# Performance work log

Hardware: AMD Instinct MI355X
Metric: run time of the kernel (lower is better)

Reference implementation:

```python
import jax, jax.numpy as jnp
import numpy as np
from jax import lax

# Config constants (DeepSeek-V2-style gate)
N_EXPERTS = 64
TOP_K = 6
N_GROUP = 8
TOPK_GROUP = 3
NORM_TOPK_PROB = True
ROUTED_SCALING_FACTOR = 1.0


def setup_inputs() -> dict:
    key = jax.random.key(0)
    k1, k2 = jax.random.split(key)
    B, S, H = 4, 8192, 2048
    hidden_states = jax.random.normal(k1, (B, S, H), dtype=jnp.float32)
    # gate kernel: (n_routed_experts, gating_dim), kaiming-uniform-ish scale
    bound = float(np.sqrt(6.0 / H))
    kernel = jax.random.uniform(k2, (N_EXPERTS, H), dtype=jnp.float32, minval=-bound, maxval=bound)
    return {"hidden_states": hidden_states, "kernel": kernel}


def reference(hidden_states, kernel):
    B, S, H = hidden_states.shape
    T = B * S
    flat = hidden_states.reshape(T, H).astype(jnp.float32)
    # logits: [T, E]  (x @ W^T, as in DeepSeek gate)
    logits = jnp.einsum("th,eh->te", flat, kernel.astype(jnp.float32))
    scores = jax.nn.softmax(logits, axis=-1)  # [T, E]

    # group_limited_greedy: pick best TOPK_GROUP groups per token, mask the rest
    per_group = N_EXPERTS // N_GROUP
    group_scores = scores.reshape(T, N_GROUP, per_group).max(axis=-1)  # [T, G]
    top_group_idx = lax.top_k(group_scores, TOPK_GROUP)[1]  # [T, topk_group]
    group_mask = jnp.zeros((T, N_GROUP), dtype=scores.dtype)
    group_mask = group_mask.at[jnp.arange(T)[:, None], top_group_idx].set(1.0)
    score_mask = jnp.repeat(group_mask[:, :, None], per_group, axis=2).reshape(T, N_EXPERTS)
    masked_scores = jnp.where(score_mask.astype(bool), scores, 0.0)
    topk_weight, _ = lax.top_k(masked_scores, TOP_K)  # [T, top_k]

    if TOP_K > 1 and NORM_TOPK_PROB:
        denom = jnp.sum(topk_weight, axis=-1, keepdims=True) + 1e-20
        topk_weight = topk_weight / denom
    else:
        topk_weight = topk_weight * ROUTED_SCALING_FACTOR
    return topk_weight
```

## Files before the change

### kernel.cpp

```cpp
#include <hip/hip_runtime.h>
#include <hip/hip_bf16.h>


#define HD 2048
#define NE 64
#define NCH 16
#define BUFB 32768

typedef __attribute__((ext_vector_type(4))) float f4;
typedef __attribute__((ext_vector_type(8))) short s8;
typedef __attribute__((ext_vector_type(8))) _Float16 h8;
typedef __attribute__((ext_vector_type(4))) float accv;
typedef unsigned short u16;

__device__ __forceinline__ void split8h(const f4 v0, const f4 v1, s8& h, s8& l) {
  #pragma unroll
  for (int i = 0; i < 8; ++i) {
    float a = (i < 4) ? v0[i] : v1[i - 4];
    _Float16 hh = (_Float16)a;
    float r = a - (float)hh;
    _Float16 ll = (_Float16)r;
    h[i] = __builtin_bit_cast(short, hh);
    l[i] = __builtin_bit_cast(short, ll);
  }
}

__device__ __forceinline__ accv mfma3(s8 ah, s8 al, s8 bh, s8 bl, accv t) {
  h8 AH = __builtin_bit_cast(h8, ah);
  h8 AL = __builtin_bit_cast(h8, al);
  h8 BH = __builtin_bit_cast(h8, bh);
  h8 BL = __builtin_bit_cast(h8, bl);
  t = __builtin_amdgcn_mfma_f32_16x16x32_f16(AH, BH, t, 0, 0, 0);
  t = __builtin_amdgcn_mfma_f32_16x16x32_f16(AH, BL, t, 0, 0, 0);
  t = __builtin_amdgcn_mfma_f32_16x16x32_f16(AL, BH, t, 0, 0, 0);
  return t;
}

__device__ __forceinline__ void epilogue64(const float* v, float* op) {
  float gm[8];
  #pragma unroll
  for (int g = 0; g < 8; ++g) {
    float mx = v[g * 8];
    #pragma unroll
    for (int j = 1; j < 8; ++j) mx = fmaxf(mx, v[g * 8 + j]);
    gm[g] = mx;
  }
  unsigned selmask = 0u;
  #pragma unroll
  for (int itg = 0; itg < 3; ++itg) {
    float best = gm[0];
    #pragma unroll
    for (int g = 1; g < 8; ++g) best = fmaxf(best, gm[g]);
    int bi = 7;
    #pragma unroll
    for (int g = 6; g >= 0; --g)
      if (gm[g] == best) bi = g;
    selmask |= (1u << bi);
    #pragma unroll
    for (int g = 0; g < 8; ++g) gm[g] = (g == bi) ? -3.0e38f : gm[g];
  }
  float t0 = -3.0e38f, t1 = -3.0e38f, t2 = -3.0e38f;
  float t3 = -3.0e38f, t4 = -3.0e38f, t5 = -3.0e38f;
  #pragma unroll
  for (int g = 0; g < 8; ++g) {
    const bool sel = (selmask >> g) & 1u;
    #pragma unroll
    for (int j = 0; j < 8; ++j) {
      float x = sel ? v[g * 8 + j] : -3.0e38f;
      float mm;
      mm = fmaxf(t0, x); x = fminf(t0, x); t0 = mm;
      mm = fmaxf(t1, x); x = fminf(t1, x); t1 = mm;
      mm = fmaxf(t2, x); x = fminf(t2, x); t2 = mm;
      mm = fmaxf(t3, x); x = fminf(t3, x); t3 = mm;
      mm = fmaxf(t4, x); x = fminf(t4, x); t4 = mm;
      t5 = fmaxf(t5, x);
    }
  }
  float e0 = 1.0f;
  float e1 = __expf(t1 - t0);
  float e2 = __expf(t2 - t0);
  float e3 = __expf(t3 - t0);
  float e4 = __expf(t4 - t0);
  float e5 = __expf(t5 - t0);
  float sum = e0 + e1 + e2 + e3 + e4 + e5;
  float inv = 1.0f / sum;
  op[0] = e0 * inv; op[1] = e1 * inv; op[2] = e2 * inv;
  op[3] = e3 * inv; op[4] = e4 * inv; op[5] = e5 * inv;
}

__global__ __launch_bounds__(64) void cvtW2(const float* __restrict__ Wf,
                                            u16* __restrict__ Wh,
                                            u16* __restrict__ Wl) {
  int i = (blockIdx.x * 64 + threadIdx.x) * 8;
  f4 v0 = *(const f4*)(Wf + i);
  f4 v1 = *(const f4*)(Wf + i + 4);
  s8 h, l;
  split8h(v0, v1, h, l);
  *(s8*)((short*)Wh + i) = h;
  *(s8*)((short*)Wl + i) = l;
}

template <bool PRE>
__global__ __launch_bounds__(512, 4) void gateF(
    const float* __restrict__ X, const float* __restrict__ Wf,
    const u16* __restrict__ Wh, const u16* __restrict__ Wl,
    float* __restrict__ out) {
  __shared__ __align__(16) unsigned char smem[2 * BUFB];

  const int tid = threadIdx.x;
  const int lane = tid & 63;
  const int w = tid >> 6;
  const int ec = lane & 15;
  const int kg = lane >> 4;
  const int tok0 = blockIdx.x * 128;

  const float* pA = X + (size_t)(tok0 + w * 16 + ec) * HD + kg * 8;

  const int sw = w >> 1, spl = w & 1;
  const u16* Wsrc = spl ? Wl : Wh;
  const size_t wsrcb = (size_t)ec * HD + sw * 32 + kg * 8;
  const int sdstb = sw * 8192 + spl * 4096 + lane * 16;

  accv acc[4];
  #pragma unroll
  for (int f = 0; f < 4; ++f) acc[f] = (accv){0.f, 0.f, 0.f, 0.f};

  f4 ar[4][2];

  if constexpr (PRE) {
    #pragma unroll
    for (int j = 0; j < 4; ++j) {
      const size_t o = wsrcb + (size_t)j * 16 * HD;
      __builtin_amdgcn_global_load_lds((const unsigned int*)(Wsrc + o),
                                       (unsigned int*)(smem + sdstb + j * 1024), 16, 0, 0);
    }
  } else {
    #pragma unroll
    for (int j = 0; j < 4; ++j) {
      const size_t o = wsrcb + (size_t)j * 16 * HD;
      f4 r0 = *(const f4*)(Wf + o);
      f4 r1 = *(const f4*)(Wf + o + 4);
      s8 th, tl;
      split8h(r0, r1, th, tl);
      *(s8*)(smem + sw * 8192 + j * 1024 + lane * 16) = th;
      *(s8*)(smem + sw * 8192 + 4096 + j * 1024 + lane * 16) = tl;
    }
  }
  __builtin_amdgcn_sched_barrier(0);
  #pragma unroll
  for (int st = 0; st < 4; ++st) {
    ar[st][0] = *(const f4*)(pA + st * 32);
    ar[st][1] = *(const f4*)(pA + st * 32 + 4);
  }
  __builtin_amdgcn_sched_barrier(0);
  if constexpr (PRE) {
    asm volatile("s_waitcnt vmcnt(8) lgkmcnt(0)");
  } else {
    asm volatile("s_waitcnt lgkmcnt(0)");
  }
  __builtin_amdgcn_s_barrier();
  __builtin_amdgcn_sched_barrier(0);


  for (int c = 0; c < NCH; ++c) {
    const unsigned char* rb = smem + (c & 1) * BUFB;
    unsigned char* wb = smem + ((c + 1) & 1) * BUFB;
    const bool do_stage = (c + 1 < NCH);

    f4 q0[4], q1[4];
    if (do_stage) {
      if constexpr (PRE) {
        #pragma unroll
        for (int j = 0; j < 4; ++j) {
          const size_t o = wsrcb + (size_t)j * 16 * HD + (size_t)(c + 1) * 128;
          __builtin_amdgcn_global_load_lds((const unsigned int*)(Wsrc + o),
                                           (unsigned int*)(wb + sdstb + j * 1024), 16, 0, 0);
        }
      } else {
        #pragma unroll
        for (int j = 0; j < 4; ++j) {
          const size_t o = wsrcb + (size_t)j * 16 * HD + (size_t)(c + 1) * 128;
          q0[j] = *(const f4*)(Wf + o);
          q1[j] = *(const f4*)(Wf + o + 4);
        }
      }
    }
    __builtin_amdgcn_sched_barrier(0);

    #pragma unroll
    for (int st = 0; st < 4; ++st) {
      const int t = c * 4 + st;
      s8 ah, al;
      split8h(ar[st][0], ar[st][1], ah, al);
      const int tn = (t + 4 < 64) ? (t + 4) : 63;
      ar[st][0] = *(const f4*)(pA + tn * 32);
      ar[st][1] = *(const f4*)(pA + tn * 32 + 4);
      #pragma unroll
      for (int f = 0; f < 4; ++f) {
        const unsigned char* bp = rb + st * 8192 + f * 1024 + lane * 16;
        s8 bh = *(const s8*)(bp);
        s8 bl = *(const s8*)(bp + 4096);
        acc[f] = mfma3(ah, al, bh, bl, acc[f]);
      }
    }

    if (do_stage) {
      if constexpr (!PRE) {
        #pragma unroll
        for (int j = 0; j < 4; ++j) {
          s8 th, tl;
          split8h(q0[j], q1[j], th, tl);
          *(s8*)(wb + sw * 8192 + j * 1024 + lane * 16) = th;
          *(s8*)(wb + sw * 8192 + 4096 + j * 1024 + lane * 16) = tl;
        }
      }
    }
    if (do_stage) {
      __builtin_amdgcn_sched_barrier(0);
      if constexpr (PRE) {
        asm volatile("s_waitcnt vmcnt(8) lgkmcnt(0)");
      } else {
        asm volatile("s_waitcnt lgkmcnt(0)");
      }
      __builtin_amdgcn_s_barrier();
      __builtin_amdgcn_sched_barrier(0);
    }
  }

  __syncthreads();
  float* lf = (float*)smem + w * 1088;
  #pragma unroll
  for (int f = 0; f < 4; ++f)
    #pragma unroll
    for (int r = 0; r < 4; ++r)
      lf[(kg * 4 + r) * 68 + f * 16 + ec] = acc[f][r];

  if (lane < 16) {
    float v[64];
    #pragma unroll
    for (int i = 0; i < 16; ++i) {
      f4 q = *(const f4*)(lf + lane * 68 + 4 * i);
      v[4 * i + 0] = q.x; v[4 * i + 1] = q.y;
      v[4 * i + 2] = q.z; v[4 * i + 3] = q.w;
    }
    epilogue64(v, out + (size_t)(tok0 + w * 16 + lane) * 6);
  }
}

extern "C" void kernel_launch(void* const* d_in, const int* in_sizes, int n_in,
                              void* d_out, int out_size, void* d_ws, size_t ws_size,
                              hipStream_t stream) {
  const float* X = (const float*)d_in[0];
  const float* Wf = (const float*)d_in[1];
  float* out = (float*)d_out;
  const int T = in_sizes[0] / HD;
  const int nblk = T / 128;

  const size_t need = (size_t)NE * HD * sizeof(u16);
  if (ws_size >= 2 * need) {
    u16* Whi = (u16*)d_ws;
    u16* Wlo = Whi + (size_t)NE * HD;
    cvtW2<<<dim3(256), dim3(64), 0, stream>>>(Wf, Whi, Wlo);
    gateF<true><<<dim3(nblk), dim3(512), 0, stream>>>(X, Wf, Whi, Wlo, out);
  } else {
    gateF<false><<<dim3(nblk), dim3(512), 0, stream>>>(X, Wf, nullptr, nullptr, out);
  }
}
```

Measured before the change: 70.85 us.

## Stream activations through per-wave swizzled LDS ring via direct global-to-LDS loads

Activation tiles no longer go through register prefetch. Each wave now issues global_load_lds into a 4-slot XOR-swizzled LDS ring, three k-steps ahead, with fine-grained vmcnt waits, and reads its operands back from LDS. LDS grows to 128 KB, so occupancy is capped at 2 blocks per CU, and s_setprio is raised around the MFMA section. The aim is to free VGPRs and hide global latency better, at the cost of lower occupancy and fragile vmcnt bookkeeping. The non-PRE path also changes: each wave now writes only one half of the split weights, which looks like a behaviour change.

```diff
diff --git a/kernel.cpp b/kernel.cpp
--- a/kernel.cpp
+++ b/kernel.cpp
@@ -5,7 +5,9 @@
 #define HD 2048
 #define NE 64
 #define NCH 16
-#define BUFB 32768
+#define ABASE 0
+#define BBASE 65536
+#define BBUF 32768
 
 typedef __attribute__((ext_vector_type(4))) float f4;
 typedef __attribute__((ext_vector_type(8))) short s8;
@@ -101,11 +103,11 @@
 }
 
 template <bool PRE>
-__global__ __launch_bounds__(512, 4) void gateF(
+__global__ __launch_bounds__(512, 2) void gateF(
     const float* __restrict__ X, const float* __restrict__ Wf,
     const u16* __restrict__ Wh, const u16* __restrict__ Wl,
     float* __restrict__ out) {
-  __shared__ __align__(16) unsigned char smem[2 * BUFB];
+  __shared__ __align__(16) unsigned char smem[BBASE + 2 * BBUF];
 
   const int tid = threadIdx.x;
   const int lane = tid & 63;
@@ -114,26 +116,32 @@
   const int kg = lane >> 4;
   const int tok0 = blockIdx.x * 128;
 
-  const float* pA = X + (size_t)(tok0 + w * 16 + ec) * HD + kg * 8;
-
-  const int sw = w >> 1, spl = w & 1;
-  const u16* Wsrc = spl ? Wl : Wh;
-  const size_t wsrcb = (size_t)ec * HD + sw * 32 + kg * 8;
-  const int sdstb = sw * 8192 + spl * 4096 + lane * 16;
+  const int rowlo = lane >> 3;
+  const int colf = ((lane & 7) * 4) ^ (rowlo << 2);
+  const float* srcA0 = X + (size_t)(tok0 + w * 16 + rowlo) * HD + colf;
+  const float* srcA1 = X + (size_t)(tok0 + w * 16 + 8 + rowlo) * HD + colf;
+  unsigned char* const aring = smem + ABASE + w * 8192;
+
+  const int a0b = ec * 128 + kg * 32;
+  const int sw = (ec & 7) << 4;
+  const int rdA0 = a0b ^ sw;
+  const int rdA1 = (a0b + 16) ^ sw;
+
+  const int bst = w >> 1, bspl = w & 1;
+  const u16* WsrcB = bspl ? Wl : Wh;
+  const size_t wsrcb = (size_t)ec * HD + bst * 32 + kg * 8;
+  const int bdst = bst * 8192 + bspl * 4096 + lane * 16;
 
   accv acc[4];
   #pragma unroll
   for (int f = 0; f < 4; ++f) acc[f] = (accv){0.f, 0.f, 0.f, 0.f};
 
-  f4 ar[4][2];
-
   if constexpr (PRE) {
     #pragma unroll
-    for (int j = 0; j < 4; ++j) {
-      const size_t o = wsrcb + (size_t)j * 16 * HD;
-      __builtin_amdgcn_global_load_lds((const unsigned int*)(Wsrc + o),
-                                       (unsigned int*)(smem + sdstb + j * 1024), 16, 0, 0);
-    }
+    for (int j = 0; j < 4; ++j)
+      __builtin_amdgcn_global_load_lds(
+          (const unsigned int*)(WsrcB + wsrcb + (size_t)j * 16 * HD),
+          (unsigned int*)(smem + BBASE + bdst + j * 1024), 16, 0, 0);
   } else {
     #pragma unroll
     for (int j = 0; j < 4; ++j) {
@@ -142,40 +150,37 @@
       f4 r1 = *(const f4*)(Wf + o + 4);
       s8 th, tl;
       split8h(r0, r1, th, tl);
-      *(s8*)(smem + sw * 8192 + j * 1024 + lane * 16) = th;
-      *(s8*)(smem + sw * 8192 + 4096 + j * 1024 + lane * 16) = tl;
-    }
+      *(s8*)(smem + BBASE + bst * 8192 + bspl * 4096 + j * 1024 + lane * 16) =
+          bspl ? tl : th;
+    }
+  }
+  #pragma unroll
+  for (int st = 0; st < 3; ++st) {
+    unsigned char* ad = aring + st * 2048 + lane * 16;
+    __builtin_amdgcn_global_load_lds((const unsigned int*)(srcA0 + st * 32),
+                                     (unsigned int*)(ad), 16, 0, 0);
+    __builtin_amdgcn_global_load_lds((const unsigned int*)(srcA1 + st * 32),
+                                     (unsigned int*)(ad + 1024), 16, 0, 0);
   }
   __builtin_amdgcn_sched_barrier(0);
-  #pragma unroll
-  for (int st = 0; st < 4; ++st) {
-    ar[st][0] = *(const f4*)(pA + st * 32);
-    ar[st][1] = *(const f4*)(pA + st * 32 + 4);
-  }
-  __builtin_amdgcn_sched_barrier(0);
-  if constexpr (PRE) {
-    asm volatile("s_waitcnt vmcnt(8) lgkmcnt(0)");
-  } else {
-    asm volatile("s_waitcnt lgkmcnt(0)");
-  }
+  asm volatile("s_waitcnt vmcnt(6) lgkmcnt(0)" ::: "memory");
   __builtin_amdgcn_s_barrier();
   __builtin_amdgcn_sched_barrier(0);
 
-
   for (int c = 0; c < NCH; ++c) {
-    const unsigned char* rb = smem + (c & 1) * BUFB;
-    unsigned char* wb = smem + ((c + 1) & 1) * BUFB;
+    const unsigned char* rb = smem + BBASE + (c & 1) * BBUF;
+    unsigned char* wbB = smem + BBASE + ((c + 1) & 1) * BBUF + bdst;
     const bool do_stage = (c + 1 < NCH);
 
     f4 q0[4], q1[4];
     if (do_stage) {
       if constexpr (PRE) {
         #pragma unroll
-        for (int j = 0; j < 4; ++j) {
-          const size_t o = wsrcb + (size_t)j * 16 * HD + (size_t)(c + 1) * 128;
-          __builtin_amdgcn_global_load_lds((const unsigned int*)(Wsrc + o),
-                                           (unsigned int*)(wb + sdstb + j * 1024), 16, 0, 0);
-        }
+        for (int j = 0; j < 4; ++j)
+          __builtin_amdgcn_global_load_lds(
+              (const unsigned int*)(WsrcB + wsrcb + (size_t)j * 16 * HD +
+                                    (size_t)(c + 1) * 128),
+              (unsigned int*)(wbB + j * 1024), 16, 0, 0);
       } else {
         #pragma unroll
         for (int j = 0; j < 4; ++j) {
@@ -188,20 +193,37 @@
     __builtin_amdgcn_sched_barrier(0);
 
     #pragma unroll
-    for (int st = 0; st < 4; ++st) {
-      const int t = c * 4 + st;
+    for (int st4 = 0; st4 < 4; ++st4) {
+      const int t = c * 4 + st4;
+      if constexpr (PRE) {
+        if (st4 < 3 && c < NCH - 1) {
+          asm volatile("s_waitcnt vmcnt(8)" ::: "memory");
+        } else {
+          asm volatile("s_waitcnt vmcnt(4)" ::: "memory");
+        }
+      } else {
+        asm volatile("s_waitcnt vmcnt(0)" ::: "memory");
+      }
+      const unsigned char* slot = aring + (t & 3) * 2048;
+      f4 v0 = *(const f4*)(slot + rdA0);
+      f4 v1 = *(const f4*)(slot + rdA1);
+      const int tn = (t + 3 < 64) ? (t + 3) : 63;
+      unsigned char* ad = aring + (tn & 3) * 2048 + lane * 16;
+      __builtin_amdgcn_global_load_lds((const unsigned int*)(srcA0 + tn * 32),
+                                       (unsigned int*)(ad), 16, 0, 0);
+      __builtin_amdgcn_global_load_lds((const unsigned int*)(srcA1 + tn * 32),
+                                       (unsigned int*)(ad + 1024), 16, 0, 0);
+      __builtin_amdgcn_s_setprio(1);
       s8 ah, al;
-      split8h(ar[st][0], ar[st][1], ah, al);
-      const int tn = (t + 4 < 64) ? (t + 4) : 63;
-      ar[st][0] = *(const f4*)(pA + tn * 32);
-      ar[st][1] = *(const f4*)(pA + tn * 32 + 4);
+      split8h(v0, v1, ah, al);
       #pragma unroll
       for (int f = 0; f < 4; ++f) {
-        const unsigned char* bp = rb + st * 8192 + f * 1024 + lane * 16;
+        const unsigned char* bp = rb + st4 * 8192 + f * 1024 + lane * 16;
         s8 bh = *(const s8*)(bp);
         s8 bl = *(const s8*)(bp + 4096);
         acc[f] = mfma3(ah, al, bh, bl, acc[f]);
       }
+      __builtin_amdgcn_s_setprio(0);
     }
 
     if (do_stage) {
@@ -210,17 +232,16 @@
         for (int j = 0; j < 4; ++j) {
           s8 th, tl;
           split8h(q0[j], q1[j], th, tl);
-          *(s8*)(wb + sw * 8192 + j * 1024 + lane * 16) = th;
-          *(s8*)(wb + sw * 8192 + 4096 + j * 1024 + lane * 16) = tl;
+          *(s8*)(wbB + j * 1024) = bspl ? tl : th;
         }
       }
     }
     if (do_stage) {
       __builtin_amdgcn_sched_barrier(0);
       if constexpr (PRE) {
-        asm volatile("s_waitcnt vmcnt(8) lgkmcnt(0)");
+        asm volatile("s_waitcnt vmcnt(8) lgkmcnt(0)" ::: "memory");
       } else {
-        asm volatile("s_waitcnt lgkmcnt(0)");
+        asm volatile("s_waitcnt lgkmcnt(0)" ::: "memory");
       }
       __builtin_amdgcn_s_barrier();
       __builtin_amdgcn_sched_barrier(0);
```

Result: faster. 57.08 us (-19.4%).
